# Kernel optimization log

Measured on AMD Instinct MI355X. Metric: run time of the kernel, lower is better.

## Reference

```python
import jax, jax.numpy as jnp
import numpy as np

N_NODES = 100000
N_EDGES = 1600000
F_IN = 128
HID = 128
N_CLASSES = 32
N_GRAPHS = 512


def _seg_mean(vals, idx, num_segments):
    s = jax.ops.segment_sum(vals, idx, num_segments=num_segments)
    cnt = jax.ops.segment_sum(jnp.ones((vals.shape[0],), vals.dtype), idx, num_segments=num_segments)
    return s / jnp.maximum(cnt, 1.0)[:, None]


def _sage_conv(x, src, dst, Wl, bl, Wr):
    # PyG SAGEConv(mean): out = lin_l(mean_{j in N(i)} x_j) + lin_r(x_i); lin_l has bias, lin_r does not.
    agg = _seg_mean(x[src], dst, N_NODES)          # gather + scatter-mean  [N, d]
    return agg @ Wl.T + bl + x @ Wr.T              # [N, H]


def setup_inputs() -> dict:
    key = jax.random.key(0)
    ks = jax.random.split(key, 16)
    x = jax.random.normal(ks[0], (N_NODES, F_IN), dtype=jnp.float32)
    edge_index = jax.random.randint(ks[1], (2, N_EDGES), 0, N_NODES, dtype=jnp.int64)
    batch = jnp.sort(jax.random.randint(ks[2], (N_NODES,), 0, N_GRAPHS, dtype=jnp.int64))
    sc = 0.05
    params = {
        'Wl0': jax.random.normal(ks[3], (HID, F_IN), jnp.float32) * sc,
        'bl0': jnp.zeros((HID,), jnp.float32),
        'Wr0': jax.random.normal(ks[4], (HID, F_IN), jnp.float32) * sc,
        'Wl1': jax.random.normal(ks[5], (HID, HID), jnp.float32) * sc,
        'bl1': jnp.zeros((HID,), jnp.float32),
        'Wr1': jax.random.normal(ks[6], (HID, HID), jnp.float32) * sc,
        'Wl2': jax.random.normal(ks[7], (HID, HID), jnp.float32) * sc,
        'bl2': jnp.zeros((HID,), jnp.float32),
        'Wr2': jax.random.normal(ks[8], (HID, HID), jnp.float32) * sc,
        'Wlin': jax.random.normal(ks[9], (N_CLASSES, HID), jnp.float32) * sc,
        'blin': jnp.zeros((N_CLASSES,), jnp.float32),
    }
    return {'x': x, 'edge_index': edge_index, 'batch': batch, **params}


def reference(x, edge_index, batch, Wl0, bl0, Wr0, Wl1, bl1, Wr1, Wl2, bl2, Wr2, Wlin, blin):
    src, dst = edge_index[0], edge_index[1]
    # GraphSAGE backbone: relu between layers, no act after last (out_channels set); dropout=identity in eval.
    h = jax.nn.relu(_sage_conv(x, src, dst, Wl0, bl0, Wr0))
    h = jax.nn.relu(_sage_conv(h, src, dst, Wl1, bl1, Wr1))
    h = _sage_conv(h, src, dst, Wl2, bl2, Wr2)
    # global_mean_pool over batch index -> [n_graphs, HID]
    g = _seg_mean(h, batch, N_GRAPHS)
    return g @ Wlin.T + blin  # [n_graphs, n_classes]
```

## Files before the change

### kernel.cpp

```cpp
#include <hip/hip_runtime.h>
#include <hip/hip_bf16.h>


typedef __attribute__((ext_vector_type(8))) short short8v;
typedef __attribute__((ext_vector_type(4))) float f32x4;

#define RK_CH 12544
#define RK_NS 64

__device__ __forceinline__ unsigned short f2bf(float f) {
    __hip_bfloat16 h = __float2bfloat16(f);
    return *reinterpret_cast<unsigned short*>(&h);
}
__device__ __forceinline__ float bf_lo(unsigned u) { return __uint_as_float(u << 16); }
__device__ __forceinline__ float bf_hi(unsigned u) { return __uint_as_float(u & 0xffff0000u); }
__device__ __forceinline__ unsigned packbf(float lo, float hi) {
    return ((unsigned)f2bf(hi) << 16) | f2bf(lo);
}


__launch_bounds__(256)
__global__ void rank_hist_kernel(const int* __restrict__ dst,
                                 unsigned short* __restrict__ rank16,
                                 unsigned short* __restrict__ counts16,
                                 int nE, int nChunk, int es) {
    __shared__ unsigned cnt[RK_CH];
    int s = blockIdx.x / nChunk;
    int c = blockIdx.x % nChunk;
    int lo = c * RK_CH;
    for (int i = threadIdx.x; i < RK_CH; i += 256) cnt[i] = 0u;
    __syncthreads();

    int ebeg = s * es;
    int eend = ebeg + es; if (eend > nE) eend = nE;

    if (ebeg < eend) {
        if ((((size_t)dst) & 15) == 0) {
            int nvec = (eend - ebeg) >> 2;
            for (int g = threadIdx.x; g < nvec; g += 256) {
                int e = ebeg + g * 4;
                int4 d4 = *(const int4*)&dst[e];
                unsigned dc;
                dc = (unsigned)(d4.x - lo);
                if (dc < RK_CH) rank16[e]     = (unsigned short)atomicAdd(&cnt[dc], 1u);
                dc = (unsigned)(d4.y - lo);
                if (dc < RK_CH) rank16[e + 1] = (unsigned short)atomicAdd(&cnt[dc], 1u);
                dc = (unsigned)(d4.z - lo);
                if (dc < RK_CH) rank16[e + 2] = (unsigned short)atomicAdd(&cnt[dc], 1u);
                dc = (unsigned)(d4.w - lo);
                if (dc < RK_CH) rank16[e + 3] = (unsigned short)atomicAdd(&cnt[dc], 1u);
            }
            for (int e = ebeg + (nvec << 2) + threadIdx.x; e < eend; e += 256) {
                unsigned dc = (unsigned)(dst[e] - lo);
                if (dc < RK_CH) rank16[e] = (unsigned short)atomicAdd(&cnt[dc], 1u);
            }
        } else {
            for (int e = ebeg + threadIdx.x; e < eend; e += 256) {
                unsigned dc = (unsigned)(dst[e] - lo);
                if (dc < RK_CH) rank16[e] = (unsigned short)atomicAdd(&cnt[dc], 1u);
            }
        }
    }
    __syncthreads();
    size_t base = ((size_t)(c * RK_NS + s)) * RK_CH;
    for (int i = threadIdx.x; i < RK_CH; i += 256)
        counts16[base + i] = (unsigned short)cnt[i];
}

__global__ void seg_offsets_kernel(unsigned short* __restrict__ counts16,
                                   int* __restrict__ deg, int n) {
    int d = blockIdx.x * blockDim.x + threadIdx.x;
    if (d >= n) return;
    int c = d / RK_CH;
    int i = d - c * RK_CH;
    size_t base = ((size_t)c * RK_NS) * RK_CH + i;
    unsigned run = 0;
    for (int s = 0; s < RK_NS; ++s) {
        size_t idx = base + (size_t)s * RK_CH;
        unsigned v = counts16[idx];
        counts16[idx] = (unsigned short)run;
        run += v;
    }
    deg[d] = (int)run;
}

__global__ void scan1_kernel(const int* __restrict__ deg, int* __restrict__ rowptr,
                             int* __restrict__ bsum, int n) {
    __shared__ int s[1024];
    int lid = threadIdx.x;
    int i = blockIdx.x * 1024 + lid;
    int v = (i < n) ? deg[i] : 0;
    s[lid] = v;
    __syncthreads();
    #pragma unroll
    for (int off = 1; off < 1024; off <<= 1) {
        int t = (lid >= off) ? s[lid - off] : 0;
        __syncthreads();
        s[lid] += t;
        __syncthreads();
    }
    if (i < n) rowptr[i] = s[lid] - v;
    if (lid == 0) bsum[blockIdx.x] = s[1023];
}

__global__ void scan2_kernel(int* __restrict__ bsum, int nb) {
    __shared__ int s[1024];
    int lid = threadIdx.x;
    int v = (lid < nb) ? bsum[lid] : 0;
    s[lid] = v;
    __syncthreads();
    #pragma unroll
    for (int off = 1; off < 1024; off <<= 1) {
        int t = (lid >= off) ? s[lid - off] : 0;
        __syncthreads();
        s[lid] += t;
        __syncthreads();
    }
    if (lid < nb) bsum[lid] = s[lid] - v;
}

__global__ void scan3_kernel(int* __restrict__ rowptr, const int* __restrict__ bsum,
                             int n, int nE) {
    int i = blockIdx.x * blockDim.x + threadIdx.x;
    if (i < n) rowptr[i] += bsum[i >> 10];
    if (i == 0) rowptr[n] = nE;
}

__global__ void scatter2_kernel(const int* __restrict__ src, const int* __restrict__ dst,
                                const unsigned short* __restrict__ rank16,
                                const unsigned short* __restrict__ counts16,
                                const int* __restrict__ rowptr,
                                int* __restrict__ esrc, int nE, int es, int lo, int hi) {
    int e = blockIdx.x * blockDim.x + threadIdx.x;
    if (e >= nE) return;
    int d = dst[e];
    if (d < lo || d >= hi) return;
    int s = e / es;
    int c = d / RK_CH;
    int i = d - c * RK_CH;
    int pos = rowptr[d] + (int)counts16[((size_t)(c * RK_NS + s)) * RK_CH + i]
                        + (int)rank16[e];
    esrc[pos] = src[e];
}


__global__ void cvt_kernel(const float* __restrict__ in, unsigned short* __restrict__ out, int n4) {
    int i = blockIdx.x * blockDim.x + threadIdx.x;
    if (i < n4) {
        float4 v = ((const float4*)in)[i];
        ushort4 o;
        o.x = f2bf(v.x); o.y = f2bf(v.y); o.z = f2bf(v.z); o.w = f2bf(v.w);
        ((ushort4*)out)[i] = o;
    }
}

__global__ void cvt6_kernel(const float* __restrict__ w0, const float* __restrict__ w1,
                            const float* __restrict__ w2, const float* __restrict__ w3,
                            const float* __restrict__ w4, const float* __restrict__ w5,
                            unsigned short* __restrict__ o0, unsigned short* __restrict__ o1,
                            unsigned short* __restrict__ o2, unsigned short* __restrict__ o3,
                            unsigned short* __restrict__ o4, unsigned short* __restrict__ o5,
                            int n4) {
    const float* in; unsigned short* out;
    switch (blockIdx.y) {
        case 0: in = w0; out = o0; break;
        case 1: in = w1; out = o1; break;
        case 2: in = w2; out = o2; break;
        case 3: in = w3; out = o3; break;
        case 4: in = w4; out = o4; break;
        default: in = w5; out = o5; break;
    }
    int i = blockIdx.x * blockDim.x + threadIdx.x;
    if (i < n4) {
        float4 v = ((const float4*)in)[i];
        ushort4 o;
        o.x = f2bf(v.x); o.y = f2bf(v.y); o.z = f2bf(v.z); o.w = f2bf(v.w);
        ((ushort4*)out)[i] = o;
    }
}


__global__ void aggregate_kernel(const unsigned short* __restrict__ h,
                                 const int* __restrict__ rowptr,
                                 const int* __restrict__ esrc,
                                 unsigned short* __restrict__ agg, int n) {
    int wave = (blockIdx.x * blockDim.x + threadIdx.x) >> 6;
    int lane = threadIdx.x & 63;
    if (wave >= n) return;
    int beg = rowptr[wave], end = rowptr[wave + 1];
    int q  = lane >> 4;
    int c0 = (lane & 15) * 8;
    float s0=0.f,s1=0.f,s2=0.f,s3=0.f,s4=0.f,s5=0.f,s6=0.f,s7=0.f;
    int j = beg + q;
    for (; j + 4 < end; j += 8) {
        int r0 = esrc[j], r1 = esrc[j + 4];
        uint4 v0 = *(const uint4*)&h[(size_t)r0 * 128 + c0];
        uint4 v1 = *(const uint4*)&h[(size_t)r1 * 128 + c0];
        s0 += bf_lo(v0.x); s1 += bf_hi(v0.x); s2 += bf_lo(v0.y); s3 += bf_hi(v0.y);
        s4 += bf_lo(v0.z); s5 += bf_hi(v0.z); s6 += bf_lo(v0.w); s7 += bf_hi(v0.w);
        s0 += bf_lo(v1.x); s1 += bf_hi(v1.x); s2 += bf_lo(v1.y); s3 += bf_hi(v1.y);
        s4 += bf_lo(v1.z); s5 += bf_hi(v1.z); s6 += bf_lo(v1.w); s7 += bf_hi(v1.w);
    }
    if (j < end) {
        int r0 = esrc[j];
        uint4 v0 = *(const uint4*)&h[(size_t)r0 * 128 + c0];
        s0 += bf_lo(v0.x); s1 += bf_hi(v0.x); s2 += bf_lo(v0.y); s3 += bf_hi(v0.y);
        s4 += bf_lo(v0.z); s5 += bf_hi(v0.z); s6 += bf_lo(v0.w); s7 += bf_hi(v0.w);
    }
    s0 += __shfl_xor(s0, 16); s0 += __shfl_xor(s0, 32);
    s1 += __shfl_xor(s1, 16); s1 += __shfl_xor(s1, 32);
    s2 += __shfl_xor(s2, 16); s2 += __shfl_xor(s2, 32);
    s3 += __shfl_xor(s3, 16); s3 += __shfl_xor(s3, 32);
    s4 += __shfl_xor(s4, 16); s4 += __shfl_xor(s4, 32);
    s5 += __shfl_xor(s5, 16); s5 += __shfl_xor(s5, 32);
    s6 += __shfl_xor(s6, 16); s6 += __shfl_xor(s6, 32);
    s7 += __shfl_xor(s7, 16); s7 += __shfl_xor(s7, 32);
    if (lane < 16) {
        int cnt = end - beg;
        float inv = 1.0f / (float)(cnt > 1 ? cnt : 1);
        uint4 o;
        o.x = packbf(s0 * inv, s1 * inv);
        o.y = packbf(s2 * inv, s3 * inv);
        o.z = packbf(s4 * inv, s5 * inv);
        o.w = packbf(s6 * inv, s7 * inv);
        *(uint4*)&agg[(size_t)wave * 128 + c0] = o;
    }
}


__launch_bounds__(256)
__global__ void sage_gemm_mfma(const unsigned short* __restrict__ A,
                               const unsigned short* __restrict__ H,
                               const unsigned short* __restrict__ Wl,
                               const unsigned short* __restrict__ Wr,
                               const float* __restrict__ bl,
                               unsigned short* __restrict__ out, int n, int relu) {
    int tid  = threadIdx.x;
    int lane = tid & 63;
    int w    = tid >> 6;
    int wm   = w >> 1, wn = w & 1;
    int br   = blockIdx.x * 128 + wm * 64;
    int bc   = wn * 64;
    int lrow = lane & 15;
    int lk   = (lane >> 4) * 8;

    f32x4 acc[4][4] = {};

    #pragma unroll
    for (int half = 0; half < 2; ++half) {
        const unsigned short* X = half ? H : A;
        const unsigned short* W = half ? Wr : Wl;
        const unsigned short* xp[4];
        const unsigned short* wp[4];
        #pragma unroll
        for (int mb = 0; mb < 4; ++mb) {
            int r = br + mb * 16 + lrow;
            if (r >= n) r = n - 1;
            xp[mb] = X + (size_t)r * 128 + lk;
        }
        #pragma unroll
        for (int nb = 0; nb < 4; ++nb)
            wp[nb] = W + (size_t)(bc + nb * 16 + lrow) * 128 + lk;

        #pragma unroll
        for (int ks = 0; ks < 4; ++ks) {
            short8v a[4], b[4];
            #pragma unroll
            for (int mb = 0; mb < 4; ++mb) a[mb] = *(const short8v*)(xp[mb] + ks * 32);
            #pragma unroll
            for (int nb = 0; nb < 4; ++nb) b[nb] = *(const short8v*)(wp[nb] + ks * 32);
            #pragma unroll
            for (int mb = 0; mb < 4; ++mb)
                #pragma unroll
                for (int nb = 0; nb < 4; ++nb)
                    acc[mb][nb] = __builtin_amdgcn_mfma_f32_16x16x32_bf16(
                        a[mb], b[nb], acc[mb][nb], 0, 0, 0);
        }
    }

    int ccol  = lane & 15;
    int crow4 = (lane >> 4) * 4;
    float bv[4];
    #pragma unroll
    for (int nb = 0; nb < 4; ++nb) bv[nb] = bl[bc + nb * 16 + ccol];

    #pragma unroll
    for (int mb = 0; mb < 4; ++mb) {
        #pragma unroll
        for (int r = 0; r < 4; ++r) {
            int row = br + mb * 16 + crow4 + r;
            if (row < n) {
                #pragma unroll
                for (int nb = 0; nb < 4; ++nb) {
                    int col = bc + nb * 16 + ccol;
                    float v = acc[mb][nb][r] + bv[nb];
                    if (relu && v < 0.f) v = 0.f;
                    out[(size_t)row * 128 + col] = f2bf(v);
                }
            }
        }
    }
}


__device__ __forceinline__ int lbound(const int* __restrict__ a, int n, int v) {
    int lo = 0, hi = n;
    while (lo < hi) { int m = (lo + hi) >> 1; if (a[m] < v) lo = m + 1; else hi = m; }
    return lo;
}

__launch_bounds__(1024)
__global__ void pool_kernel(const unsigned short* __restrict__ h, const int* __restrict__ batch,
                            float* __restrict__ g, int n) {
    __shared__ float red[16][128];
    int b  = blockIdx.x;
    int rg = threadIdx.x >> 6;
    int cp = threadIdx.x & 63;
    int lo = lbound(batch, n, b);
    int hi = lbound(batch, n, b + 1);
    float s0 = 0.f, s1 = 0.f;
    for (int i = lo + rg; i < hi; i += 16) {
        unsigned v = *(const unsigned*)&h[(size_t)i * 128 + cp * 2];
        s0 += bf_lo(v); s1 += bf_hi(v);
    }
    red[rg][cp * 2]     = s0;
    red[rg][cp * 2 + 1] = s1;
    __syncthreads();
    #pragma unroll
    for (int off = 8; off >= 1; off >>= 1) {
        if (rg < off) {
            red[rg][cp * 2]     += red[rg + off][cp * 2];
            red[rg][cp * 2 + 1] += red[rg + off][cp * 2 + 1];
        }
        __syncthreads();
    }
    if (rg == 0) {
        int cnt = hi - lo;
        float inv = 1.0f / (float)(cnt > 1 ? cnt : 1);
        g[(size_t)b * 128 + cp * 2]     = red[0][cp * 2] * inv;
        g[(size_t)b * 128 + cp * 2 + 1] = red[0][cp * 2 + 1] * inv;
    }
}

__global__ void final_kernel(const float* __restrict__ g, const float* __restrict__ Wlin,
                             const float* __restrict__ blin, float* __restrict__ out, int total) {
    int gid = blockIdx.x * blockDim.x + threadIdx.x;
    if (gid >= total) return;
    int b = gid >> 5;
    int j = gid & 31;
    const float* gr = &g[(size_t)b * 128];
    const float* wr = &Wlin[(size_t)j * 128];
    float s = blin[j];
    #pragma unroll 4
    for (int c = 0; c < 128; ++c) s += gr[c] * wr[c];
    out[gid] = s;
}

extern "C" void kernel_launch(void* const* d_in, const int* in_sizes, int n_in,
                              void* d_out, int out_size, void* d_ws, size_t ws_size,
                              hipStream_t stream) {
    const float* x      = (const float*)d_in[0];
    const int*   eidx   = (const int*)d_in[1];
    const int*   batch  = (const int*)d_in[2];
    const float* Wl[3]  = {(const float*)d_in[3], (const float*)d_in[6], (const float*)d_in[9]};
    const float* bl[3]  = {(const float*)d_in[4], (const float*)d_in[7], (const float*)d_in[10]};
    const float* Wr[3]  = {(const float*)d_in[5], (const float*)d_in[8], (const float*)d_in[11]};
    const float* Wlin   = (const float*)d_in[12];
    const float* blin   = (const float*)d_in[13];
    float* out = (float*)d_out;

    const int N = in_sizes[0] / 128;
    const int E = in_sizes[1] / 2;
    const int G = out_size / 32;

    const int* esrc_in = eidx;
    const int* edst_in = eidx + E;

    char* w = (char*)d_ws;
    auto carve = [&](size_t bytes) { char* p = w; w += (bytes + 255) & ~(size_t)255; return p; };
    unsigned short* xbf  = (unsigned short*)carve((size_t)N * 128 * 2);
    unsigned short* hA   = (unsigned short*)carve((size_t)N * 128 * 2);
    unsigned short* hB   = (unsigned short*)carve((size_t)N * 128 * 2);
    unsigned short* agg  = (unsigned short*)carve((size_t)N * 128 * 2);
    unsigned short* Wbf[6];
    for (int i = 0; i < 6; ++i) Wbf[i] = (unsigned short*)carve((size_t)128 * 128 * 2);
    float* g      = (float*)carve((size_t)G * 128 * 4);
    int*   deg    = (int*)carve((size_t)N * 4);
    int*   rowptr = (int*)carve((size_t)(N + 1) * 4);
    int*   bsum   = (int*)carve(1024 * 4);
    int*   esrc   = (int*)carve((size_t)E * 4);
    unsigned short* rank16   = (unsigned short*)carve((size_t)E * 2);
    int nChunk = (N + RK_CH - 1) / RK_CH;
    unsigned short* counts16 = (unsigned short*)carve((size_t)nChunk * RK_NS * RK_CH * 2);
    (void)ws_size; (void)n_in;

    int es = (((E + RK_NS - 1) / RK_NS) + 3) & ~3;
    hipLaunchKernelGGL(rank_hist_kernel, dim3(nChunk * RK_NS), dim3(256), 0, stream,
                       edst_in, rank16, counts16, E, nChunk, es);
    int ngrid = (N + 255) / 256;
    hipLaunchKernelGGL(seg_offsets_kernel, dim3(ngrid), dim3(256), 0, stream,
                       counts16, deg, N);
    int nchunks = (N + 1023) / 1024;
    hipLaunchKernelGGL(scan1_kernel, dim3(nchunks), dim3(1024), 0, stream, deg, rowptr, bsum, N);
    hipLaunchKernelGGL(scan2_kernel, dim3(1), dim3(1024), 0, stream, bsum, nchunks);
    hipLaunchKernelGGL(scan3_kernel, dim3(ngrid), dim3(256), 0, stream, rowptr, bsum, N, E);
    int egrid = (E + 255) / 256;
    const int NPASS = 2;
    int chunk = (N + NPASS - 1) / NPASS;
    for (int p = 0; p < NPASS; ++p) {
        int lo = p * chunk;
        int hi = lo + chunk < N ? lo + chunk : N;
        hipLaunchKernelGGL(scatter2_kernel, dim3(egrid), dim3(256), 0, stream,
                           esrc_in, edst_in, rank16, counts16, rowptr, esrc, E, es, lo, hi);
    }

    int x4 = N * 128 / 4;
    hipLaunchKernelGGL(cvt_kernel, dim3((x4 + 255) / 256), dim3(256), 0, stream, x, xbf, x4);
    int w4 = 128 * 128 / 4;
    hipLaunchKernelGGL(cvt6_kernel, dim3((w4 + 255) / 256, 6), dim3(256), 0, stream,
                       Wl[0], Wr[0], Wl[1], Wr[1], Wl[2], Wr[2],
                       Wbf[0], Wbf[1], Wbf[2], Wbf[3], Wbf[4], Wbf[5], w4);

    int agrid = (N + 3) / 4;
    int ggrid = (N + 127) / 128;
    const unsigned short* hin = xbf;
    unsigned short* houts[3] = {hA, hB, hA};
    for (int l = 0; l < 3; ++l) {
        hipLaunchKernelGGL(aggregate_kernel, dim3(agrid), dim3(256), 0, stream,
                           hin, rowptr, esrc, agg, N);
        hipLaunchKernelGGL(sage_gemm_mfma, dim3(ggrid), dim3(256), 0, stream,
                           agg, hin, Wbf[2*l], Wbf[2*l+1], bl[l], houts[l], N, (l < 2) ? 1 : 0);
        hin = houts[l];
    }

    hipLaunchKernelGGL(pool_kernel, dim3(G), dim3(1024), 0, stream, hin, batch, g, N);
    int fgrid = (out_size + 255) / 256;
    hipLaunchKernelGGL(final_kernel, dim3(fgrid), dim3(256), 0, stream, g, Wlin, blin, out, out_size);
}
```

Baseline: 398.0 us.

## Fuse neighbor mean aggregation into SAGE GEMM via shared-memory tile

The separate aggregation kernel is merged into the MFMA GEMM kernel. Each block first gathers and averages neighbor features for its 128 nodes, writing them into LDS in an MFMA-friendly fragment layout, then runs the Wl product from LDS and the Wr product from global memory. This removes the write and re-read of the N×128 aggregate buffer and one launch per layer. The cost is lower gather parallelism: 782 blocks of 4 waves, each wave serially processing 32 nodes, plus 32KB of LDS per block that limits occupancy. The gather loop is also unrolled to four edges per iteration.

Measured after the change: 589.6 us. 1.48x slower.

```diff
diff --git a/kernel.cpp b/kernel.cpp
--- a/kernel.cpp
+++ b/kernel.cpp
@@ -180,64 +180,82 @@
 }
 
 
-__global__ void aggregate_kernel(const unsigned short* __restrict__ h,
-                                 const int* __restrict__ rowptr,
-                                 const int* __restrict__ esrc,
-                                 unsigned short* __restrict__ agg, int n) {
-    int wave = (blockIdx.x * blockDim.x + threadIdx.x) >> 6;
-    int lane = threadIdx.x & 63;
-    if (wave >= n) return;
-    int beg = rowptr[wave], end = rowptr[wave + 1];
-    int q  = lane >> 4;
-    int c0 = (lane & 15) * 8;
-    float s0=0.f,s1=0.f,s2=0.f,s3=0.f,s4=0.f,s5=0.f,s6=0.f,s7=0.f;
-    int j = beg + q;
-    for (; j + 4 < end; j += 8) {
-        int r0 = esrc[j], r1 = esrc[j + 4];
-        uint4 v0 = *(const uint4*)&h[(size_t)r0 * 128 + c0];
-        uint4 v1 = *(const uint4*)&h[(size_t)r1 * 128 + c0];
-        s0 += bf_lo(v0.x); s1 += bf_hi(v0.x); s2 += bf_lo(v0.y); s3 += bf_hi(v0.y);
-        s4 += bf_lo(v0.z); s5 += bf_hi(v0.z); s6 += bf_lo(v0.w); s7 += bf_hi(v0.w);
-        s0 += bf_lo(v1.x); s1 += bf_hi(v1.x); s2 += bf_lo(v1.y); s3 += bf_hi(v1.y);
-        s4 += bf_lo(v1.z); s5 += bf_hi(v1.z); s6 += bf_lo(v1.w); s7 += bf_hi(v1.w);
-    }
-    if (j < end) {
-        int r0 = esrc[j];
-        uint4 v0 = *(const uint4*)&h[(size_t)r0 * 128 + c0];
-        s0 += bf_lo(v0.x); s1 += bf_hi(v0.x); s2 += bf_lo(v0.y); s3 += bf_hi(v0.y);
-        s4 += bf_lo(v0.z); s5 += bf_hi(v0.z); s6 += bf_lo(v0.w); s7 += bf_hi(v0.w);
-    }
-    s0 += __shfl_xor(s0, 16); s0 += __shfl_xor(s0, 32);
-    s1 += __shfl_xor(s1, 16); s1 += __shfl_xor(s1, 32);
-    s2 += __shfl_xor(s2, 16); s2 += __shfl_xor(s2, 32);
-    s3 += __shfl_xor(s3, 16); s3 += __shfl_xor(s3, 32);
-    s4 += __shfl_xor(s4, 16); s4 += __shfl_xor(s4, 32);
-    s5 += __shfl_xor(s5, 16); s5 += __shfl_xor(s5, 32);
-    s6 += __shfl_xor(s6, 16); s6 += __shfl_xor(s6, 32);
-    s7 += __shfl_xor(s7, 16); s7 += __shfl_xor(s7, 32);
-    if (lane < 16) {
-        int cnt = end - beg;
-        float inv = 1.0f / (float)(cnt > 1 ? cnt : 1);
-        uint4 o;
-        o.x = packbf(s0 * inv, s1 * inv);
-        o.y = packbf(s2 * inv, s3 * inv);
-        o.z = packbf(s4 * inv, s5 * inv);
-        o.w = packbf(s6 * inv, s7 * inv);
-        *(uint4*)&agg[(size_t)wave * 128 + c0] = o;
-    }
-}
-
+#define ACC8(v) do { \
+    s0 += bf_lo((v).x); s1 += bf_hi((v).x); s2 += bf_lo((v).y); s3 += bf_hi((v).y); \
+    s4 += bf_lo((v).z); s5 += bf_hi((v).z); s6 += bf_lo((v).w); s7 += bf_hi((v).w); } while (0)
 
 __launch_bounds__(256)
-__global__ void sage_gemm_mfma(const unsigned short* __restrict__ A,
-                               const unsigned short* __restrict__ H,
-                               const unsigned short* __restrict__ Wl,
-                               const unsigned short* __restrict__ Wr,
-                               const float* __restrict__ bl,
-                               unsigned short* __restrict__ out, int n, int relu) {
+__global__ void sage_fused_kernel(const unsigned short* __restrict__ H,
+                                  const int* __restrict__ rowptr,
+                                  const int* __restrict__ esrc,
+                                  const unsigned short* __restrict__ Wl,
+                                  const unsigned short* __restrict__ Wr,
+                                  const float* __restrict__ bl,
+                                  unsigned short* __restrict__ out, int n, int relu) {
+    __shared__ unsigned short aggT[128 * 128];
     int tid  = threadIdx.x;
     int lane = tid & 63;
     int w    = tid >> 6;
+
+    {
+        int q     = lane >> 4;
+        int li    = lane & 15;
+        int c0    = li * 8;
+        int rbase = w * 32;
+        int nodeb = blockIdx.x * 128 + rbase;
+        for (int rr = 0; rr < 32; ++rr) {
+            int node = nodeb + rr;
+            float s0=0.f,s1=0.f,s2=0.f,s3=0.f,s4=0.f,s5=0.f,s6=0.f,s7=0.f;
+            int cnt = 0;
+            if (node < n) {
+                int beg = rowptr[node], end = rowptr[node + 1];
+                cnt = end - beg;
+                int j = beg + q;
+                for (; j + 12 < end; j += 16) {
+                    int r0 = esrc[j], r1 = esrc[j + 4], r2 = esrc[j + 8], r3 = esrc[j + 12];
+                    uint4 v0 = *(const uint4*)&H[(size_t)r0 * 128 + c0];
+                    uint4 v1 = *(const uint4*)&H[(size_t)r1 * 128 + c0];
+                    uint4 v2 = *(const uint4*)&H[(size_t)r2 * 128 + c0];
+                    uint4 v3 = *(const uint4*)&H[(size_t)r3 * 128 + c0];
+                    ACC8(v0); ACC8(v1); ACC8(v2); ACC8(v3);
+                }
+                for (; j + 4 < end; j += 8) {
+                    int r0 = esrc[j], r1 = esrc[j + 4];
+                    uint4 v0 = *(const uint4*)&H[(size_t)r0 * 128 + c0];
+                    uint4 v1 = *(const uint4*)&H[(size_t)r1 * 128 + c0];
+                    ACC8(v0); ACC8(v1);
+                }
+                if (j < end) {
+                    int r0 = esrc[j];
+                    uint4 v0 = *(const uint4*)&H[(size_t)r0 * 128 + c0];
+                    ACC8(v0);
+                }
+                s0 += __shfl_xor(s0, 16); s0 += __shfl_xor(s0, 32);
+                s1 += __shfl_xor(s1, 16); s1 += __shfl_xor(s1, 32);
+                s2 += __shfl_xor(s2, 16); s2 += __shfl_xor(s2, 32);
+                s3 += __shfl_xor(s3, 16); s3 += __shfl_xor(s3, 32);
+                s4 += __shfl_xor(s4, 16); s4 += __shfl_xor(s4, 32);
+                s5 += __shfl_xor(s5, 16); s5 += __shfl_xor(s5, 32);
+                s6 += __shfl_xor(s6, 16); s6 += __shfl_xor(s6, 32);
+                s7 += __shfl_xor(s7, 16); s7 += __shfl_xor(s7, 32);
+            }
+            if (lane < 16) {
+                float inv = 1.0f / (float)(cnt > 1 ? cnt : 1);
+                int r  = rbase + rr;
+                int ks = lane >> 2;
+                int g  = lane & 3;
+                int slot = (((r >> 4) * 4 + ks) * 64 + ((r & 15) | (g << 4))) * 8;
+                uint4 o;
+                o.x = packbf(s0 * inv, s1 * inv);
+                o.y = packbf(s2 * inv, s3 * inv);
+                o.z = packbf(s4 * inv, s5 * inv);
+                o.w = packbf(s6 * inv, s7 * inv);
+                *(uint4*)&aggT[slot] = o;
+            }
+        }
+    }
+    __syncthreads();
+
     int wm   = w >> 1, wn = w & 1;
     int br   = blockIdx.x * 128 + wm * 64;
     int bc   = wn * 64;
@@ -246,22 +264,39 @@
 
     f32x4 acc[4][4] = {};
 
-    #pragma unroll
-    for (int half = 0; half < 2; ++half) {
-        const unsigned short* X = half ? H : A;
-        const unsigned short* W = half ? Wr : Wl;
+    {
+        const unsigned short* wp[4];
+        #pragma unroll
+        for (int nb = 0; nb < 4; ++nb)
+            wp[nb] = Wl + (size_t)(bc + nb * 16 + lrow) * 128 + lk;
+        #pragma unroll
+        for (int ks = 0; ks < 4; ++ks) {
+            short8v a[4], b[4];
+            #pragma unroll
+            for (int mb = 0; mb < 4; ++mb)
+                a[mb] = *(const short8v*)&aggT[(((wm * 4 + mb) * 4 + ks) * 64 + lane) * 8];
+            #pragma unroll
+            for (int nb = 0; nb < 4; ++nb) b[nb] = *(const short8v*)(wp[nb] + ks * 32);
+            #pragma unroll
+            for (int mb = 0; mb < 4; ++mb)
+                #pragma unroll
+                for (int nb = 0; nb < 4; ++nb)
+                    acc[mb][nb] = __builtin_amdgcn_mfma_f32_16x16x32_bf16(
+                        a[mb], b[nb], acc[mb][nb], 0, 0, 0);
+        }
+    }
+    {
         const unsigned short* xp[4];
         const unsigned short* wp[4];
         #pragma unroll
         for (int mb = 0; mb < 4; ++mb) {
             int r = br + mb * 16 + lrow;
             if (r >= n) r = n - 1;
-            xp[mb] = X + (size_t)r * 128 + lk;
+            xp[mb] = H + (size_t)r * 128 + lk;
         }
         #pragma unroll
         for (int nb = 0; nb < 4; ++nb)
-            wp[nb] = W + (size_t)(bc + nb * 16 + lrow) * 128 + lk;
-
+            wp[nb] = Wr + (size_t)(bc + nb * 16 + lrow) * 128 + lk;
         #pragma unroll
         for (int ks = 0; ks < 4; ++ks) {
             short8v a[4], b[4];
@@ -381,7 +416,6 @@
     unsigned short* xbf  = (unsigned short*)carve((size_t)N * 128 * 2);
     unsigned short* hA   = (unsigned short*)carve((size_t)N * 128 * 2);
     unsigned short* hB   = (unsigned short*)carve((size_t)N * 128 * 2);
-    unsigned short* agg  = (unsigned short*)carve((size_t)N * 128 * 2);
     unsigned short* Wbf[6];
     for (int i = 0; i < 6; ++i) Wbf[i] = (unsigned short*)carve((size_t)128 * 128 * 2);
     float* g      = (float*)carve((size_t)G * 128 * 4);
@@ -421,15 +455,12 @@
                        Wl[0], Wr[0], Wl[1], Wr[1], Wl[2], Wr[2],
                        Wbf[0], Wbf[1], Wbf[2], Wbf[3], Wbf[4], Wbf[5], w4);
 
-    int agrid = (N + 3) / 4;
     int ggrid = (N + 127) / 128;
     const unsigned short* hin = xbf;
     unsigned short* houts[3] = {hA, hB, hA};
     for (int l = 0; l < 3; ++l) {
-        hipLaunchKernelGGL(aggregate_kernel, dim3(agrid), dim3(256), 0, stream,
-                           hin, rowptr, esrc, agg, N);
-        hipLaunchKernelGGL(sage_gemm_mfma, dim3(ggrid), dim3(256), 0, stream,
-                           agg, hin, Wbf[2*l], Wbf[2*l+1], bl[l], houts[l], N, (l < 2) ? 1 : 0);
+        hipLaunchKernelGGL(sage_fused_kernel, dim3(ggrid), dim3(256), 0, stream,
+                           hin, rowptr, esrc, Wbf[2*l], Wbf[2*l+1], bl[l], houts[l], N, (l < 2) ? 1 : 0);
         hin = houts[l];
     }
 
```
